# Kernel tuning notes

Measured on AMD Instinct MI355X. Metric: run time of the kernel, lower is better.

The kernel has to match this reference:

```python
import jax, jax.numpy as jnp
import numpy as np

S, L, D = 512, 128, 256        # sents, sent_len, embedding_dim (= out_hidden, skip_rnn)
V, E_V, E_D = 50000, 10000, 64  # vocab, entity vocab, entity dim
B, P = 128, 16                  # batch examples, positions per example
H2, F = D // 2, 256             # attn hidden, feature_size


def setup_inputs() -> dict:
    key = jax.random.key(0)
    ks = jax.random.split(key, 16)
    emb = jax.random.normal(ks[0], (V, D), jnp.float32) * 0.02
    emb = emb.at[0].set(0.0)  # padding_idx=0
    ent_emb = jax.random.normal(ks[1], (E_V, E_D), jnp.float32) * 0.02
    ent_emb = ent_emb.at[0].set(0.0)
    x = jax.random.randint(ks[2], (S, L), 0, V)
    ents = jax.random.randint(ks[3], (B, 2), 0, E_V)
    spos = jax.random.randint(ks[4], (B, P, 2), 0, L)  # valid for both sent(<S) and tok(<L) axes
    tpos = jax.random.randint(ks[5], (B, P, 2), 0, L)
    attw_W = jax.random.normal(ks[6], (H2, D), jnp.float32) / np.sqrt(D)
    attw_b = jnp.zeros((H2,), jnp.float32)
    attw2_W = jax.random.normal(ks[7], (1, H2), jnp.float32) / np.sqrt(H2)
    FEAT = 2 * D + 2 * E_D
    cond_W = jax.random.normal(ks[8], (F, FEAT), jnp.float32) / np.sqrt(FEAT)
    cond_b = jnp.zeros((F,), jnp.float32)
    lin_W = jax.random.normal(ks[9], (2, F), jnp.float32) / np.sqrt(F)
    lin_b = jnp.zeros((2,), jnp.float32)
    return {"x": x, "ents": ents, "spos": spos, "tpos": tpos,
            "emb": emb, "ent_emb": ent_emb,
            "attw_W": attw_W, "attw_b": attw_b, "attw2_W": attw2_W,
            "cond_W": cond_W, "cond_b": cond_b, "lin_W": lin_W, "lin_b": lin_b}


def _attn_pool(h, attw_W, attw_b, attw2_W):
    # h: [B, P, D]  ->  [B, D]
    energy = jnp.tanh(jnp.einsum('bpd,hd->bph', h, attw_W) + attw_b)
    logits = jnp.einsum('bph,oh->bpo', energy, attw2_W)[..., 0]   # [B, P]
    w = jax.nn.softmax(logits, axis=1)
    return jnp.einsum('bp,bpd->bd', w, h)


def reference(x, ents, spos, tpos, emb, ent_emb, attw_W, attw_b, attw2_W,
              cond_W, cond_b, lin_W, lin_b):
    sent_hiddens = emb[x]                                  # [S, L, D] (skip_rnn path)
    s_h = sent_hiddens[spos[..., 0], spos[..., 1]]         # [B, P, D] ragged gather (batched)
    t_h = sent_hiddens[tpos[..., 0], tpos[..., 1]]         # [B, P, D]
    s_pool = _attn_pool(s_h, attw_W, attw_b, attw2_W)      # [B, D]
    t_pool = _attn_pool(t_h, attw_W, attw_b, attw2_W)      # [B, D]
    e_embs = ent_emb[ents].reshape(ents.shape[0], -1)      # [B, 2*E_D]
    feats = jnp.concatenate([s_pool, t_pool, e_embs], axis=-1)  # [B, 2D+2E_D]
    condensed = feats @ cond_W.T + cond_b                  # [B, F]
    score = jnp.tanh(condensed) @ lin_W.T + lin_b          # [B, 2]
    return score
```

## Files before the change

### kernel.cpp

```cpp
#include <hip/hip_runtime.h>

#define S_ 512
#define L_ 128
#define D_ 256
#define B_ 128
#define P_ 16
#define H2_ 128
#define F_ 256
#define FEAT_ 640
#define ED_ 64
#define SH_STRIDE 264
#define LP_STRIDE 33

__device__ float gpool[B_][2][D_];
__device__ int   gcount[B_];

__global__ __launch_bounds__(512) void fused_kernel(
    const int* __restrict__ x, const int* __restrict__ ents,
    const int* __restrict__ spos, const int* __restrict__ tpos,
    const float* __restrict__ emb, const float* __restrict__ ent_emb,
    const float* __restrict__ attw_W, const float* __restrict__ attw_b,
    const float* __restrict__ attw2_W,
    const float* __restrict__ cond_W, const float* __restrict__ cond_b,
    const float* __restrict__ lin_W, const float* __restrict__ lin_b,
    float* __restrict__ out)
{
    const int bid = blockIdx.x;
    const int b = bid >> 1, pool = bid & 1;
    const int t = threadIdx.x;

    __shared__ float sh[P_ * SH_STRIDE];
    __shared__ float lp[P_ * LP_STRIDE];
    __shared__ float logits[P_];
    __shared__ float wts[P_];
    volatile __shared__ float vdummy[256];
    __shared__ int sflag;
    __shared__ float feats[FEAT_];
    __shared__ float part[F_];
    __shared__ float r0s[4], r1s[4];

    {
        const int r = t >> 5, sub = t & 31;
        const int* pos = pool ? tpos : spos;
        const int si  = pos[(b * P_ + r) * 2 + 0];
        const int ti  = pos[(b * P_ + r) * 2 + 1];
        const int tok = x[si * L_ + ti];
        const float4* row = (const float4*)(emb + (size_t)tok * D_);
        float4 v0 = row[sub];
        float4 v1 = row[sub + 32];
        float* base = &sh[r * SH_STRIDE];
        *(float4*)&base[sub * 4]       = v0;
        *(float4*)&base[128 + sub * 4] = v1;
    }
    __syncthreads();

    {
        const int pb = (t >> 8) * 8, tl = t & 255;
        const int hp = tl >> 3, dh = tl & 7;
        const int h0 = hp * 4;
        const float4* W4 = (const float4*)attw_W;

        float acc[4][8];
        #pragma unroll
        for (int qq = 0; qq < 4; ++qq)
            #pragma unroll
            for (int p = 0; p < 8; ++p) acc[qq][p] = 0.f;

        float4 nxt[4];
        #pragma unroll
        for (int qq = 0; qq < 4; ++qq) nxt[qq] = W4[(h0 + qq) * 64 + dh];

        for (int c = 0; c < 8; ++c) {
            float4 a[4];
            #pragma unroll
            for (int qq = 0; qq < 4; ++qq) a[qq] = nxt[qq];
            if (c < 7) {
                #pragma unroll
                for (int qq = 0; qq < 4; ++qq)
                    nxt[qq] = W4[(h0 + qq) * 64 + 8 * (c + 1) + dh];
            }
            const int d = (8 * c + dh) * 4;
            #pragma unroll
            for (int p = 0; p < 8; ++p) {
                float4 s = *(const float4*)&sh[(pb + p) * SH_STRIDE + d];
                #pragma unroll
                for (int qq = 0; qq < 4; ++qq)
                    acc[qq][p] += a[qq].x * s.x + a[qq].y * s.y + a[qq].z * s.z + a[qq].w * s.w;
            }
        }

        #pragma unroll
        for (int qq = 0; qq < 4; ++qq) {
            #pragma unroll
            for (int j = 0; j < 4; ++j) {
                float lo = acc[qq][j],     olo = __shfl_xor(lo, 4, 64);
                float hi = acc[qq][j + 4], ohi = __shfl_xor(hi, 4, 64);
                acc[qq][j] = (dh & 4) ? (hi + ohi) : (lo + olo);
            }
            #pragma unroll
            for (int j = 0; j < 2; ++j) {
                float lo = acc[qq][j],     olo = __shfl_xor(lo, 2, 64);
                float hi = acc[qq][j + 2], ohi = __shfl_xor(hi, 2, 64);
                acc[qq][j] = (dh & 2) ? (hi + ohi) : (lo + olo);
            }
            {
                float lo = acc[qq][0], olo = __shfl_xor(lo, 1, 64);
                float hi = acc[qq][1], ohi = __shfl_xor(hi, 1, 64);
                acc[qq][0] = (dh & 1) ? (hi + ohi) : (lo + olo);
            }
        }
        const float b0 = attw_b[h0],     b1 = attw_b[h0 + 1];
        const float b2 = attw_b[h0 + 2], b3 = attw_b[h0 + 3];
        const float w0 = attw2_W[h0],     w1 = attw2_W[h0 + 1];
        const float w2 = attw2_W[h0 + 2], w3 = attw2_W[h0 + 3];
        float v = tanhf(acc[0][0] + b0) * w0 + tanhf(acc[1][0] + b1) * w1
                + tanhf(acc[2][0] + b2) * w2 + tanhf(acc[3][0] + b3) * w3;
        lp[(pb + dh) * LP_STRIDE + hp] = v;
    }
    __syncthreads();

    if (t < 256) {
        const int p = t >> 4, g = t & 15;
        float s = lp[p * LP_STRIDE + 2 * g] + lp[p * LP_STRIDE + 2 * g + 1];
        #pragma unroll
        for (int m = 1; m <= 8; m <<= 1) s += __shfl_xor(s, m, 64);
        if (g == 0) logits[p] = s;
    }
    __syncthreads();

    if (t < 16) {
        float l = logits[t];
        float m = l;
        for (int mm = 8; mm >= 1; mm >>= 1) m = fmaxf(m, __shfl_xor(m, mm, 64));
        float e = expf(l - m);
        float ssum = e;
        for (int mm = 8; mm >= 1; mm >>= 1) ssum += __shfl_xor(ssum, mm, 64);
        wts[t] = e / ssum;
    }
    __syncthreads();

    if (t < 256) {
        float acc = 0.f;
        #pragma unroll
        for (int p = 0; p < P_; ++p) acc += wts[p] * sh[p * SH_STRIDE + t];
        float old = atomicExch(&gpool[b][pool][t], acc);
        vdummy[t] = old;
    }
    __syncthreads();

    if (t == 0) {
        float f = vdummy[0];
        int addv = 1 + (int)(f * 0.0f);
        sflag = atomicAdd(&gcount[b], addv);
    }
    __syncthreads();
    if (sflag == 0) return;
    if (t == 0) atomicExch(&gcount[b], 0);

    {
        const int pp = t >> 8, d = t & 255;
        feats[pp * 256 + d] = atomicAdd(&gpool[b][pp][d], 0.0f);
    }
    if (t < 128) {
        const int e = ents[b * 2 + (t >> 6)];
        feats[512 + t] = ent_emb[(size_t)e * ED_ + (t & 63)];
    }
    __syncthreads();

    {
        const int g = t >> 4, sub = t & 15;
        #pragma unroll
        for (int k = 0; k < 8; ++k) {
            const int r = g + 32 * k;
            const float4* wrow = (const float4*)(cond_W + (size_t)r * FEAT_);
            float4 w[10];
            #pragma unroll
            for (int j = 0; j < 10; ++j) w[j] = wrow[j * 16 + sub];
            float acc = 0.f;
            #pragma unroll
            for (int j = 0; j < 10; ++j) {
                const float* fp = &feats[(j * 16 + sub) * 4];
                acc += w[j].x * fp[0] + w[j].y * fp[1] + w[j].z * fp[2] + w[j].w * fp[3];
            }
            #pragma unroll
            for (int m = 1; m <= 8; m <<= 1) acc += __shfl_xor(acc, m, 64);
            if (sub == 0) part[r] = acc + cond_b[r];
        }
    }
    __syncthreads();

    if (t < 256) {
        const float tv = tanhf(part[t]);
        float v0 = tv * lin_W[t];
        float v1 = tv * lin_W[256 + t];
        #pragma unroll
        for (int m = 32; m >= 1; m >>= 1) {
            v0 += __shfl_xor(v0, m, 64);
            v1 += __shfl_xor(v1, m, 64);
        }
        if ((t & 63) == 0) { r0s[t >> 6] = v0; r1s[t >> 6] = v1; }
    }
    __syncthreads();
    if (t == 0) {
        out[b * 2 + 0] = r0s[0] + r0s[1] + r0s[2] + r0s[3] + lin_b[0];
        out[b * 2 + 1] = r1s[0] + r1s[1] + r1s[2] + r1s[3] + lin_b[1];
    }
}

extern "C" void kernel_launch(void* const* d_in, const int* in_sizes, int n_in,
                              void* d_out, int out_size, void* d_ws, size_t ws_size,
                              hipStream_t stream)
{
    const int* x     = (const int*)d_in[0];
    const int* ents  = (const int*)d_in[1];
    const int* spos  = (const int*)d_in[2];
    const int* tpos  = (const int*)d_in[3];
    const float* emb     = (const float*)d_in[4];
    const float* ent_emb = (const float*)d_in[5];
    const float* attw_W  = (const float*)d_in[6];
    const float* attw_b  = (const float*)d_in[7];
    const float* attw2_W = (const float*)d_in[8];
    const float* cond_W  = (const float*)d_in[9];
    const float* cond_b  = (const float*)d_in[10];
    const float* lin_W   = (const float*)d_in[11];
    const float* lin_b   = (const float*)d_in[12];
    float* out = (float*)d_out;

    fused_kernel<<<2 * B_, 512, 0, stream>>>(
        x, ents, spos, tpos, emb, ent_emb, attw_W, attw_b, attw2_W,
        cond_W, cond_b, lin_W, lin_b, out);
}
```

Baseline: 121.6 us.

## Split condensation matvec across both pool blocks and exchange partial sums

Each of the two blocks per example now computes its own partial of the cond_W matvec over its pooled vector and its own entity embedding, then publishes a 256-float partial through global memory. The last-arriving block adds the other block's partial, the bias, and applies tanh and the final linear layer. This spreads the serialized tail matvec over both blocks instead of doing it entirely in the last one. In exchange, both blocks now read cond_W slices and do extra work before the handoff, which lengthens the pre-sync path.

```diff
diff --git a/kernel.cpp b/kernel.cpp
--- a/kernel.cpp
+++ b/kernel.cpp
@@ -12,7 +12,7 @@
 #define SH_STRIDE 264
 #define LP_STRIDE 33
 
-__device__ float gpool[B_][2][D_];
+__device__ float gpool[B_][2][F_];
 __device__ int   gcount[B_];
 
 __global__ __launch_bounds__(512) void fused_kernel(
@@ -29,15 +29,21 @@
     const int b = bid >> 1, pool = bid & 1;
     const int t = threadIdx.x;
 
-    __shared__ float sh[P_ * SH_STRIDE];
+    __shared__ __align__(16) float sh[P_ * SH_STRIDE];
     __shared__ float lp[P_ * LP_STRIDE];
     __shared__ float logits[P_];
     __shared__ float wts[P_];
+    __shared__ __align__(16) float poolv[D_];
+    __shared__ __align__(16) float ee[ED_];
+    __shared__ float part[F_];
     volatile __shared__ float vdummy[256];
     __shared__ int sflag;
-    __shared__ float feats[FEAT_];
-    __shared__ float part[F_];
     __shared__ float r0s[4], r1s[4];
+
+    if (t < 16) {
+        const int e = ents[b * 2 + pool];
+        ((float4*)ee)[t] = ((const float4*)(ent_emb + (size_t)e * ED_))[t];
+    }
 
     {
         const int r = t >> 5, sub = t & 31;
@@ -143,7 +149,39 @@
         float acc = 0.f;
         #pragma unroll
         for (int p = 0; p < P_; ++p) acc += wts[p] * sh[p * SH_STRIDE + t];
-        float old = atomicExch(&gpool[b][pool][t], acc);
+        poolv[t] = acc;
+    }
+    __syncthreads();
+
+    {
+        const int g = t >> 4, sub = t & 15;
+        const float4* pv4 = (const float4*)poolv;
+        const float4* ee4 = (const float4*)ee;
+        const float4 p0 = pv4[sub],      p1 = pv4[16 + sub];
+        const float4 p2 = pv4[32 + sub], p3 = pv4[48 + sub];
+        const float4 pe = ee4[sub];
+        #pragma unroll
+        for (int k = 0; k < 8; ++k) {
+            const int r = g + 32 * k;
+            const float4* wp = (const float4*)(cond_W + (size_t)r * FEAT_ + pool * D_);
+            const float4* we = (const float4*)(cond_W + (size_t)r * FEAT_ + 2 * D_ + pool * ED_);
+            const float4 w0 = wp[sub],      w1 = wp[16 + sub];
+            const float4 w2 = wp[32 + sub], w3 = wp[48 + sub];
+            const float4 w4v = we[sub];
+            float acc = w0.x * p0.x + w0.y * p0.y + w0.z * p0.z + w0.w * p0.w
+                      + w1.x * p1.x + w1.y * p1.y + w1.z * p1.z + w1.w * p1.w
+                      + w2.x * p2.x + w2.y * p2.y + w2.z * p2.z + w2.w * p2.w
+                      + w3.x * p3.x + w3.y * p3.y + w3.z * p3.z + w3.w * p3.w
+                      + w4v.x * pe.x + w4v.y * pe.y + w4v.z * pe.z + w4v.w * pe.w;
+            #pragma unroll
+            for (int m = 1; m <= 8; m <<= 1) acc += __shfl_xor(acc, m, 64);
+            if (sub == 0) part[r] = acc;
+        }
+    }
+    __syncthreads();
+
+    if (t < 256) {
+        float old = atomicExch(&gpool[b][pool][t], part[t]);
         vdummy[t] = old;
     }
     __syncthreads();
@@ -157,40 +195,11 @@
     if (sflag == 0) return;
     if (t == 0) atomicExch(&gcount[b], 0);
 
-    {
-        const int pp = t >> 8, d = t & 255;
-        feats[pp * 256 + d] = atomicAdd(&gpool[b][pp][d], 0.0f);
-    }
-    if (t < 128) {
-        const int e = ents[b * 2 + (t >> 6)];
-        feats[512 + t] = ent_emb[(size_t)e * ED_ + (t & 63)];
-    }
-    __syncthreads();
-
-    {
-        const int g = t >> 4, sub = t & 15;
-        #pragma unroll
-        for (int k = 0; k < 8; ++k) {
-            const int r = g + 32 * k;
-            const float4* wrow = (const float4*)(cond_W + (size_t)r * FEAT_);
-            float4 w[10];
-            #pragma unroll
-            for (int j = 0; j < 10; ++j) w[j] = wrow[j * 16 + sub];
-            float acc = 0.f;
-            #pragma unroll
-            for (int j = 0; j < 10; ++j) {
-                const float* fp = &feats[(j * 16 + sub) * 4];
-                acc += w[j].x * fp[0] + w[j].y * fp[1] + w[j].z * fp[2] + w[j].w * fp[3];
-            }
-            #pragma unroll
-            for (int m = 1; m <= 8; m <<= 1) acc += __shfl_xor(acc, m, 64);
-            if (sub == 0) part[r] = acc + cond_b[r];
-        }
-    }
-    __syncthreads();
-
-    if (t < 256) {
-        const float tv = tanhf(part[t]);
+    if (t < 256) {
+        const float cv = part[t]
+                       + atomicAdd(&gpool[b][1 - pool][t], 0.0f)
+                       + cond_b[t];
+        const float tv = tanhf(cv);
         float v0 = tv * lin_W[t];
         float v1 = tv * lin_W[256 + t];
         #pragma unroll
```

Measured after the change: 118.5 us. -2.5%, faster.
